# Performance work log

Hardware: AMD Instinct MI355X
Metric: run time of the kernel (lower is better)

Reference implementation:

```python
import jax, jax.numpy as jnp
import numpy as np

E = 8      # num_experts
R = 32     # LoRA rank
D = 1024   # in_features (d_model)
H = 4096   # out_features of fc1 (hidden)
B = 2
S = 2048
SCALING = 1.0 / R  # lora_alpha / rank with alpha=1


def setup_inputs() -> dict:
    key = jax.random.key(0)
    ks = jax.random.split(key, 9)
    def w(k, shape, scale=0.02):
        return jax.random.normal(k, shape, dtype=jnp.float32) * scale
    return {
        "x": jax.random.normal(ks[0], (B, S, D), dtype=jnp.float32),
        "router_w": w(ks[1], (E, D)),
        "router_b": jnp.zeros((E,), jnp.float32),
        "fc1_w": w(ks[2], (H, D)),
        "fc1_b": jnp.zeros((H,), jnp.float32),
        "fc2_w": w(ks[3], (D, H)),
        "fc2_b": jnp.zeros((D,), jnp.float32),
        "A_down": w(ks[4], (E, R, D)),
        "Ab_down": jnp.zeros((E, R), jnp.float32),
        "B_down": w(ks[5], (E, H, R)),
        "Bb_down": jnp.zeros((E, H), jnp.float32),
        "A_up": w(ks[6], (E, R, H)),
        "Ab_up": jnp.zeros((E, R), jnp.float32),
        "B_up": w(ks[7], (E, D, R)),
        "Bb_up": jnp.zeros((E, D), jnp.float32),
    }


def _moe_lora(x, mask, A, Ab, Bw, Bb):
    # x: [B,S,din]; mask: one-hot [B,S,E]; A: [E,R,din]; Bw: [E,dout,R]
    # rank-stage for all experts is cheap (R=32), select per token via one-hot
    h = jnp.einsum('bsd,erd->bser', x, A) + Ab          # [B,S,E,R]
    hsel = jnp.einsum('bser,bse->bsr', h, mask)          # [B,S,R]
    out = jnp.zeros(x.shape[:2] + (Bw.shape[1],), dtype=x.dtype)
    for e in range(E):  # fixed small expert count; avoids [B,S,E,dout] blowup
        out = out + mask[..., e:e + 1] * (hsel @ Bw[e].T + Bb[e])
    return out * SCALING


def reference(x, router_w, router_b, fc1_w, fc1_b, fc2_w, fc2_b,
              A_down, Ab_down, B_down, Bb_down,
              A_up, Ab_up, B_up, Bb_up):
    logits = x @ router_w.T + router_b                   # [B,S,E]
    routing = jax.nn.softmax(logits, axis=-1)
    index = jnp.argmax(logits, axis=-1)                  # top-1 expert [B,S]
    mask = jax.nn.one_hot(index, E, dtype=x.dtype)       # y_hard [B,S,E]
    expert_choice = mask - jax.lax.stop_gradient(routing) + routing
    # down: frozen fc1 + sparse LoRA (dropout layers in eval mode -> identity)
    down = x @ fc1_w.T + fc1_b + _moe_lora(x, mask, A_down, Ab_down, B_down, Bb_down)
    a = jax.nn.gelu(down, approximate=False)             # F.gelu exact
    up = a @ fc2_w.T + fc2_b + _moe_lora(a, mask, A_up, Ab_up, B_up, Bb_up)
    return up, routing, expert_choice
```

## Files before the change

### kernel.cpp

```cpp
#include <hip/hip_runtime.h>
#include <hip/hip_bf16.h>
#include <math.h>
#include <stdint.h>

#define E_ 8
#define R_ 32
#define D_ 1024
#define H_ 4096
#define NTOK 4096
#define M_MAX 5120
#define TILES_MAX 40
#define SCALING 0.03125f

typedef __attribute__((ext_vector_type(8))) __bf16 bf16x8;
typedef __attribute__((ext_vector_type(8))) unsigned short ushort8;
typedef __attribute__((ext_vector_type(4))) float floatx4;

__device__ __forceinline__ unsigned short f2b(float f) {
    union { float f; unsigned int i; } v; v.f = f;
    unsigned int x = v.i;
    x += 0x7fffu + ((x >> 16) & 1u);
    return (unsigned short)(x >> 16);
}
__device__ __forceinline__ float gelu_exact(float v) {
    return 0.5f * v * (1.0f + erff(v * 0.70710678118654752f));
}

#define GLOAD_LDS16(g, l) __builtin_amdgcn_global_load_lds( \
    (const __attribute__((address_space(1))) void*)(g),     \
    (__attribute__((address_space(3))) void*)(l), 16, 0, 0)

__global__ __launch_bounds__(256) void k_cvt_all(
    const float* __restrict__ w1, const float* __restrict__ w2,
    const float* __restrict__ Ad, const float* __restrict__ Bd,
    const float* __restrict__ Au, const float* __restrict__ Bu,
    unsigned short* __restrict__ w1b, unsigned short* __restrict__ w2b,
    unsigned short* __restrict__ Adb, unsigned short* __restrict__ Bdb,
    unsigned short* __restrict__ Aub, unsigned short* __restrict__ Bub)
{
    long g = ((long)blockIdx.x * 256 + threadIdx.x) * 8;
    const float* src; unsigned short* dst; long off;
    if      (g <  4194304L) { src = w1; dst = w1b; off = 0; }
    else if (g <  8388608L) { src = w2; dst = w2b; off = 4194304L; }
    else if (g <  8650752L) { src = Ad; dst = Adb; off = 8388608L; }
    else if (g <  9699328L) { src = Bd; dst = Bdb; off = 8650752L; }
    else if (g < 10747904L) { src = Au; dst = Aub; off = 9699328L; }
    else                    { src = Bu; dst = Bub; off = 10747904L; }
    long i = g - off;
    float4 a = *(const float4*)(src + i);
    float4 b = *(const float4*)(src + i + 4);
    ushort8 o;
    o[0] = f2b(a.x); o[1] = f2b(a.y); o[2] = f2b(a.z); o[3] = f2b(a.w);
    o[4] = f2b(b.x); o[5] = f2b(b.y); o[6] = f2b(b.z); o[7] = f2b(b.w);
    *(ushort8*)(dst + i) = o;
}

__global__ __launch_bounds__(256) void k_router(
    const float* __restrict__ x, const float* __restrict__ rw,
    const float* __restrict__ rb,
    float* __restrict__ out, int* __restrict__ idx)
{
    const int wave = threadIdx.x >> 6, lane = threadIdx.x & 63;
    const int t = blockIdx.x * 4 + wave;
    const float4* xr = (const float4*)(x + (size_t)t * D_);
    float4 xv[4];
#pragma unroll
    for (int s = 0; s < 4; ++s) xv[s] = xr[lane + 64 * s];
    float acc[E_];
#pragma unroll
    for (int e = 0; e < E_; ++e) {
        const float4* wr = (const float4*)(rw + (size_t)e * D_);
        float s = 0.f;
#pragma unroll
        for (int u = 0; u < 4; ++u) {
            float4 wv = wr[lane + 64 * u];
            s += xv[u].x * wv.x + xv[u].y * wv.y + xv[u].z * wv.z + xv[u].w * wv.w;
        }
        acc[e] = s;
    }
#pragma unroll
    for (int e = 0; e < E_; ++e) {
#pragma unroll
        for (int m = 32; m > 0; m >>= 1) acc[e] += __shfl_xor(acc[e], m, 64);
        acc[e] += rb[e];
    }
    int best = 0;
#pragma unroll
    for (int e = 1; e < E_; ++e) if (acc[e] > acc[best]) best = e;
    const float mx = acc[best];
    float pr[E_]; float se = 0.f;
#pragma unroll
    for (int e = 0; e < E_; ++e) { pr[e] = expf(acc[e] - mx); se += pr[e]; }
    const float inv = 1.f / se;
    if (lane < E_) {
        float r = pr[lane] * inv;
        out[(size_t)NTOK * D_ + (size_t)t * E_ + lane] = r;
        float maskv = (lane == best) ? 1.f : 0.f;
        out[(size_t)NTOK * D_ + (size_t)NTOK * E_ + (size_t)t * E_ + lane] = (maskv - r) + r;
    }
    if (lane == 0) idx[t] = best;
}

__global__ __launch_bounds__(256) void k_scan(
    const int* __restrict__ idx, int* __restrict__ hdr,
    int* __restrict__ tile_e, int* __restrict__ gather)
{
    __shared__ int cnt[256][E_];
    __shared__ int tot[E_], base[E_];
    const int tid = threadIdx.x;
    for (int m = tid; m < M_MAX; m += 256) gather[m] = -1;
    int c[E_];
#pragma unroll
    for (int e = 0; e < E_; ++e) c[e] = 0;
    for (int t = tid * 16; t < tid * 16 + 16; ++t) c[idx[t] & 7]++;
#pragma unroll
    for (int e = 0; e < E_; ++e) cnt[tid][e] = c[e];
    __syncthreads();
    if (tid < E_) {
        int run = 0;
        for (int i = 0; i < 256; ++i) { int v = cnt[i][tid]; cnt[i][tid] = run; run += v; }
        tot[tid] = run;
    }
    __syncthreads();
    if (tid == 0) {
        int b = 0, tp = 0;
        for (int e = 0; e < E_; ++e) {
            base[e] = b;
            int nt = (tot[e] + 127) >> 7;
            for (int k = 0; k < nt; ++k) tile_e[tp++] = e;
            b += nt << 7;
        }
        hdr[0] = b;
        hdr[1] = tp;
        for (int k = tp; k < TILES_MAX; ++k) tile_e[k] = 0;
    }
    __syncthreads();
    int p[E_];
#pragma unroll
    for (int e = 0; e < E_; ++e) p[e] = base[e] + cnt[tid][e];
    for (int t = tid * 16; t < tid * 16 + 16; ++t) { int e = idx[t] & 7; gather[p[e]++] = t; }
}

__global__ __launch_bounds__(128) void k_gather(
    const float* __restrict__ x, const int* __restrict__ gather,
    unsigned short* __restrict__ xg)
{
    const int m = blockIdx.x, tid = threadIdx.x;
    const int t = gather[m];
    ushort8* dst = (ushort8*)(xg + (size_t)m * D_);
    ushort8 o;
    if ((unsigned)t < (unsigned)NTOK) {
        const float4* src = (const float4*)(x + (size_t)t * D_);
        float4 a = src[tid * 2], b = src[tid * 2 + 1];
        o[0] = f2b(a.x); o[1] = f2b(a.y); o[2] = f2b(a.z); o[3] = f2b(a.w);
        o[4] = f2b(b.x); o[5] = f2b(b.y); o[6] = f2b(b.z); o[7] = f2b(b.w);
    } else {
        o = (ushort8)(0);
    }
    dst[tid] = o;
}

__global__ __launch_bounds__(256) void k_lora_a2(
    const unsigned short* __restrict__ A,
    const unsigned short* __restrict__ W,
    const float* __restrict__ Ab,
    const int* __restrict__ hdr, const int* __restrict__ tile_e,
    unsigned short* __restrict__ outb,
    int Ktot)
{
    const int mtile = blockIdx.y;
    int ntiles = hdr[1]; if (ntiles > TILES_MAX) ntiles = TILES_MAX;
    if (mtile >= ntiles) return;
    const int e = tile_e[mtile] & 7;
    const int m0 = mtile * 128 + blockIdx.x * 32;
    const int wave = threadIdx.x >> 6, lane = threadIdx.x & 63;
    const int q = lane >> 4, l16 = lane & 15;
    const int Ks = Ktot >> 2;
    const int kbase = wave * Ks;
    const floatx4 z4 = {0.f, 0.f, 0.f, 0.f};
    floatx4 acc[2][2] = {{z4, z4}, {z4, z4}};
    const bf16x8* A0 = (const bf16x8*)(A + (size_t)(m0 + l16) * Ktot);
    const bf16x8* A1 = (const bf16x8*)(A + (size_t)(m0 + 16 + l16) * Ktot);
    const bf16x8* W0 = (const bf16x8*)(W + ((size_t)e * 32 + l16) * Ktot);
    const bf16x8* W1 = (const bf16x8*)(W + ((size_t)e * 32 + 16 + l16) * Ktot);
    for (int k = kbase; k < kbase + Ks; k += 32) {
        int u = (k >> 3) + q;
        bf16x8 a0 = A0[u], a1 = A1[u];
        bf16x8 b0 = W0[u], b1 = W1[u];
        acc[0][0] = __builtin_amdgcn_mfma_f32_16x16x32_bf16(a0, b0, acc[0][0], 0, 0, 0);
        acc[0][1] = __builtin_amdgcn_mfma_f32_16x16x32_bf16(a0, b1, acc[0][1], 0, 0, 0);
        acc[1][0] = __builtin_amdgcn_mfma_f32_16x16x32_bf16(a1, b0, acc[1][0], 0, 0, 0);
        acc[1][1] = __builtin_amdgcn_mfma_f32_16x16x32_bf16(a1, b1, acc[1][1], 0, 0, 0);
    }
    __shared__ float red[4][32][32];
#pragma unroll
    for (int mi = 0; mi < 2; ++mi)
#pragma unroll
        for (int ni = 0; ni < 2; ++ni)
#pragma unroll
            for (int r = 0; r < 4; ++r)
                red[wave][mi * 16 + q * 4 + r][ni * 16 + l16] = acc[mi][ni][r];
    __syncthreads();
    for (int i = threadIdx.x; i < 1024; i += 256) {
        int lr = i >> 5, c = i & 31;
        float s = red[0][lr][c] + red[1][lr][c] + red[2][lr][c] + red[3][lr][c];
        outb[(size_t)(m0 + lr) * 32 + c] = f2b(SCALING * (s + Ab[e * 32 + c]));
    }
}

template <int KTOT, bool IS_FC1>
__global__ __launch_bounds__(256) void k_mlp(
    const unsigned short* __restrict__ Amat,
    const unsigned short* __restrict__ Wmat,
    const float* __restrict__ bias,
    const unsigned short* __restrict__ lora_h,
    const unsigned short* __restrict__ lora_B,
    const float* __restrict__ lora_b,
    const int* __restrict__ hdr, const int* __restrict__ tile_e,
    const int* __restrict__ gather,
    unsigned short* __restrict__ outb,
    float* __restrict__ outf,
    int NOUT)
{
    const int mtile = blockIdx.y;
    int ntiles = hdr[1]; if (ntiles > TILES_MAX) ntiles = TILES_MAX;
    if (mtile >= ntiles) return;
    const int e = tile_e[mtile] & 7;
    const int h0 = blockIdx.x * 128;
    const int m0 = mtile * 128;
    __shared__ bf16x8 As[1024];
    __shared__ bf16x8 Bs[1024];
    const int tid = threadIdx.x;
    const int lane = tid & 63;
    const int q = lane >> 4, l16 = lane & 15;
    const int wave = tid >> 6;
    const int wm = wave & 1, wn = wave >> 1;
    const floatx4 z4 = {0.f, 0.f, 0.f, 0.f};
    floatx4 acc[4][4];
#pragma unroll
    for (int mi = 0; mi < 4; ++mi)
#pragma unroll
        for (int ni = 0; ni < 4; ++ni) acc[mi][ni] = z4;

    const unsigned short* Abase = Amat + (size_t)m0 * KTOT;
    const unsigned short* Bbase = Wmat + (size_t)h0 * KTOT;

    for (int k0 = 0; k0 < KTOT; k0 += 64) {
#pragma unroll
        for (int rnd = 0; rnd < 4; ++rnd) {
            int s = rnd * 256 + tid;
            int row = s >> 3;
            int jj = (s & 7) ^ (row & 7);
            const unsigned short* ga = Abase + (size_t)row * KTOT + k0 + jj * 8;
            const unsigned short* gb = Bbase + (size_t)row * KTOT + k0 + jj * 8;
            GLOAD_LDS16(ga, As + rnd * 256 + wave * 64);
            GLOAD_LDS16(gb, Bs + rnd * 256 + wave * 64);
        }
        __syncthreads();
#pragma unroll
        for (int ka = 0; ka < 2; ++ka) {
            bf16x8 af[4], bfr[4];
#pragma unroll
            for (int mi = 0; mi < 4; ++mi) {
                int row = wm * 64 + mi * 16 + l16;
                af[mi] = As[row * 8 + ((ka * 4 + q) ^ (row & 7))];
            }
#pragma unroll
            for (int ni = 0; ni < 4; ++ni) {
                int row = wn * 64 + ni * 16 + l16;
                bfr[ni] = Bs[row * 8 + ((ka * 4 + q) ^ (row & 7))];
            }
#pragma unroll
            for (int mi = 0; mi < 4; ++mi)
#pragma unroll
                for (int ni = 0; ni < 4; ++ni)
                    acc[mi][ni] = __builtin_amdgcn_mfma_f32_16x16x32_bf16(af[mi], bfr[ni], acc[mi][ni], 0, 0, 0);
        }
        __syncthreads();
    }

    {
        bf16x8 a2[4], b2[4];
#pragma unroll
        for (int mi = 0; mi < 4; ++mi)
            a2[mi] = *(const bf16x8*)(lora_h + (size_t)(m0 + wm * 64 + mi * 16 + l16) * 32 + q * 8);
#pragma unroll
        for (int ni = 0; ni < 4; ++ni)
            b2[ni] = *(const bf16x8*)(lora_B + ((size_t)e * NOUT + h0 + wn * 64 + ni * 16 + l16) * 32 + q * 8);
#pragma unroll
        for (int mi = 0; mi < 4; ++mi)
#pragma unroll
            for (int ni = 0; ni < 4; ++ni)
                acc[mi][ni] = __builtin_amdgcn_mfma_f32_16x16x32_bf16(a2[mi], b2[ni], acc[mi][ni], 0, 0, 0);
    }

#pragma unroll
    for (int ni = 0; ni < 4; ++ni) {
        int gh = h0 + wn * 64 + ni * 16 + l16;
        float bv = bias[gh] + SCALING * lora_b[e * NOUT + gh];
#pragma unroll
        for (int mi = 0; mi < 4; ++mi) {
#pragma unroll
            for (int r = 0; r < 4; ++r) {
                int gm = m0 + wm * 64 + mi * 16 + q * 4 + r;
                float v = acc[mi][ni][r] + bv;
                if (IS_FC1) {
                    outb[(size_t)gm * NOUT + gh] = f2b(gelu_exact(v));
                } else {
                    int t = gather[gm];
                    if ((unsigned)t < (unsigned)NTOK) outf[(size_t)t * NOUT + gh] = v;
                }
            }
        }
    }
}

#define OFF_IDX      0u
#define OFF_HDR      16384u
#define OFF_TILE     16640u
#define OFF_GATHER   16896u
#define OFF_XG       37376u
#define OFF_HSELB    13144576u
#define OFF_AG       13472256u
#define OFF_HUPB     60658176u
#define OFF_W1B      60985856u
#define OFF_W2B      69374464u
#define OFF_ADB      77763072u
#define OFF_BDB      78287360u
#define OFF_AUB      80384512u
#define OFF_BUB      82481664u
#define WS_NEEDED    83005952u

extern "C" void kernel_launch(void* const* d_in, const int* in_sizes, int n_in,
                              void* d_out, int out_size, void* d_ws, size_t ws_size,
                              hipStream_t stream)
{
    (void)out_size;
    if (ws_size < (size_t)WS_NEEDED) return;
    if (n_in < 15 || in_sizes[0] != NTOK * D_ || in_sizes[3] != H_ * D_ ||
        in_sizes[5] != D_ * H_ || in_sizes[9] != E_ * H_ * R_) return;

    const float* x   = (const float*)d_in[0];
    const float* rw  = (const float*)d_in[1];
    const float* rb  = (const float*)d_in[2];
    const float* w1  = (const float*)d_in[3];
    const float* b1  = (const float*)d_in[4];
    const float* w2  = (const float*)d_in[5];
    const float* b2  = (const float*)d_in[6];
    const float* Ad  = (const float*)d_in[7];
    const float* Abd = (const float*)d_in[8];
    const float* Bd  = (const float*)d_in[9];
    const float* Bbd = (const float*)d_in[10];
    const float* Au  = (const float*)d_in[11];
    const float* Abu = (const float*)d_in[12];
    const float* Bu  = (const float*)d_in[13];
    const float* Bbu = (const float*)d_in[14];
    float* out = (float*)d_out;
    char* ws = (char*)d_ws;

    int* idx            = (int*)(ws + OFF_IDX);
    int* hdr            = (int*)(ws + OFF_HDR);
    int* tile_e         = (int*)(ws + OFF_TILE);
    int* gather         = (int*)(ws + OFF_GATHER);
    unsigned short* xg  = (unsigned short*)(ws + OFF_XG);
    unsigned short* hsb = (unsigned short*)(ws + OFF_HSELB);
    unsigned short* ag  = (unsigned short*)(ws + OFF_AG);
    unsigned short* hub = (unsigned short*)(ws + OFF_HUPB);
    unsigned short* w1b = (unsigned short*)(ws + OFF_W1B);
    unsigned short* w2b = (unsigned short*)(ws + OFF_W2B);
    unsigned short* Adb = (unsigned short*)(ws + OFF_ADB);
    unsigned short* Bdb = (unsigned short*)(ws + OFF_BDB);
    unsigned short* Aub = (unsigned short*)(ws + OFF_AUB);
    unsigned short* Bub = (unsigned short*)(ws + OFF_BUB);

    k_cvt_all<<<5376, 256, 0, stream>>>(w1, w2, Ad, Bd, Au, Bu,
                                        w1b, w2b, Adb, Bdb, Aub, Bub);

    k_router<<<NTOK / 4, 256, 0, stream>>>(x, rw, rb, out, idx);
    k_scan<<<1, 256, 0, stream>>>(idx, hdr, tile_e, gather);
    k_gather<<<M_MAX, 128, 0, stream>>>(x, gather, xg);
    k_lora_a2<<<dim3(4, TILES_MAX), 256, 0, stream>>>(xg, Adb, Abd, hdr, tile_e, hsb, D_);
    k_mlp<D_, true><<<dim3(H_ / 128, TILES_MAX), 256, 0, stream>>>(
        xg, w1b, b1, hsb, Bdb, Bbd, hdr, tile_e, gather, ag, nullptr, H_);
    k_lora_a2<<<dim3(4, TILES_MAX), 256, 0, stream>>>(ag, Aub, Abu, hdr, tile_e, hub, H_);
    k_mlp<H_, false><<<dim3(D_ / 128, TILES_MAX), 256, 0, stream>>>(
        ag, w2b, b2, hub, Bub, Bbu, hdr, tile_e, gather, nullptr, out, D_);
}
```

Baseline: 330.2 us.

## Split-K fc2, merge convert+router kernels, use tanh GELU approximation

Result: faster. 306.7 us (-7.1%).

```diff
diff --git a/kernel.cpp b/kernel.cpp
--- a/kernel.cpp
+++ b/kernel.cpp
@@ -22,46 +22,49 @@
     x += 0x7fffu + ((x >> 16) & 1u);
     return (unsigned short)(x >> 16);
 }
-__device__ __forceinline__ float gelu_exact(float v) {
-    return 0.5f * v * (1.0f + erff(v * 0.70710678118654752f));
+__device__ __forceinline__ float gelu_fast(float v) {
+    float u = v * (0.7978845608028654f + 0.0356774080857f * v * v);
+    float t = __expf(-2.f * fabsf(u));
+    float th = (1.f - t) * __builtin_amdgcn_rcpf(1.f + t);
+    th = (u >= 0.f) ? th : -th;
+    return 0.5f * v * (1.f + th);
 }
 
 #define GLOAD_LDS16(g, l) __builtin_amdgcn_global_load_lds( \
     (const __attribute__((address_space(1))) void*)(g),     \
     (__attribute__((address_space(3))) void*)(l), 16, 0, 0)
 
-__global__ __launch_bounds__(256) void k_cvt_all(
+__global__ __launch_bounds__(256) void k_prep(
     const float* __restrict__ w1, const float* __restrict__ w2,
     const float* __restrict__ Ad, const float* __restrict__ Bd,
     const float* __restrict__ Au, const float* __restrict__ Bu,
     unsigned short* __restrict__ w1b, unsigned short* __restrict__ w2b,
     unsigned short* __restrict__ Adb, unsigned short* __restrict__ Bdb,
-    unsigned short* __restrict__ Aub, unsigned short* __restrict__ Bub)
-{
-    long g = ((long)blockIdx.x * 256 + threadIdx.x) * 8;
-    const float* src; unsigned short* dst; long off;
-    if      (g <  4194304L) { src = w1; dst = w1b; off = 0; }
-    else if (g <  8388608L) { src = w2; dst = w2b; off = 4194304L; }
-    else if (g <  8650752L) { src = Ad; dst = Adb; off = 8388608L; }
-    else if (g <  9699328L) { src = Bd; dst = Bdb; off = 8650752L; }
-    else if (g < 10747904L) { src = Au; dst = Aub; off = 9699328L; }
-    else                    { src = Bu; dst = Bub; off = 10747904L; }
-    long i = g - off;
-    float4 a = *(const float4*)(src + i);
-    float4 b = *(const float4*)(src + i + 4);
-    ushort8 o;
-    o[0] = f2b(a.x); o[1] = f2b(a.y); o[2] = f2b(a.z); o[3] = f2b(a.w);
-    o[4] = f2b(b.x); o[5] = f2b(b.y); o[6] = f2b(b.z); o[7] = f2b(b.w);
-    *(ushort8*)(dst + i) = o;
-}
-
-__global__ __launch_bounds__(256) void k_router(
+    unsigned short* __restrict__ Aub, unsigned short* __restrict__ Bub,
     const float* __restrict__ x, const float* __restrict__ rw,
     const float* __restrict__ rb,
     float* __restrict__ out, int* __restrict__ idx)
 {
+    if (blockIdx.x < 5376) {
+        long g = ((long)blockIdx.x * 256 + threadIdx.x) * 8;
+        const float* src; unsigned short* dst; long off;
+        if      (g <  4194304L) { src = w1; dst = w1b; off = 0; }
+        else if (g <  8388608L) { src = w2; dst = w2b; off = 4194304L; }
+        else if (g <  8650752L) { src = Ad; dst = Adb; off = 8388608L; }
+        else if (g <  9699328L) { src = Bd; dst = Bdb; off = 8650752L; }
+        else if (g < 10747904L) { src = Au; dst = Aub; off = 9699328L; }
+        else                    { src = Bu; dst = Bub; off = 10747904L; }
+        long i = g - off;
+        float4 a = *(const float4*)(src + i);
+        float4 b = *(const float4*)(src + i + 4);
+        ushort8 o;
+        o[0] = f2b(a.x); o[1] = f2b(a.y); o[2] = f2b(a.z); o[3] = f2b(a.w);
+        o[4] = f2b(b.x); o[5] = f2b(b.y); o[6] = f2b(b.z); o[7] = f2b(b.w);
+        *(ushort8*)(dst + i) = o;
+        return;
+    }
     const int wave = threadIdx.x >> 6, lane = threadIdx.x & 63;
-    const int t = blockIdx.x * 4 + wave;
+    const int t = (blockIdx.x - 5376) * 4 + wave;
     const float4* xr = (const float4*)(x + (size_t)t * D_);
     float4 xv[4];
 #pragma unroll
@@ -208,7 +211,7 @@
     }
 }
 
-template <int KTOT, bool IS_FC1>
+template <int KTOT, bool IS_FC1, int NSPLIT>
 __global__ __launch_bounds__(256) void k_mlp(
     const unsigned short* __restrict__ Amat,
     const unsigned short* __restrict__ Wmat,
@@ -220,6 +223,7 @@
     const int* __restrict__ gather,
     unsigned short* __restrict__ outb,
     float* __restrict__ outf,
+    float* __restrict__ P,
     int NOUT)
 {
     const int mtile = blockIdx.y;
@@ -228,6 +232,9 @@
     const int e = tile_e[mtile] & 7;
     const int h0 = blockIdx.x * 128;
     const int m0 = mtile * 128;
+    const bool extras = (NSPLIT == 1) || (blockIdx.z == 0);
+    const int Kslice = KTOT / NSPLIT;
+    const int kstart = blockIdx.z * Kslice;
     __shared__ bf16x8 As[1024];
     __shared__ bf16x8 Bs[1024];
     const int tid = threadIdx.x;
@@ -245,7 +252,7 @@
     const unsigned short* Abase = Amat + (size_t)m0 * KTOT;
     const unsigned short* Bbase = Wmat + (size_t)h0 * KTOT;
 
-    for (int k0 = 0; k0 < KTOT; k0 += 64) {
+    for (int k0 = kstart; k0 < kstart + Kslice; k0 += 64) {
 #pragma unroll
         for (int rnd = 0; rnd < 4; ++rnd) {
             int s = rnd * 256 + tid;
@@ -279,7 +286,7 @@
         __syncthreads();
     }
 
-    {
+    if (extras) {
         bf16x8 a2[4], b2[4];
 #pragma unroll
         for (int mi = 0; mi < 4; ++mi)
@@ -297,7 +304,7 @@
 #pragma unroll
     for (int ni = 0; ni < 4; ++ni) {
         int gh = h0 + wn * 64 + ni * 16 + l16;
-        float bv = bias[gh] + SCALING * lora_b[e * NOUT + gh];
+        float bv = extras ? (bias[gh] + SCALING * lora_b[e * NOUT + gh]) : 0.f;
 #pragma unroll
         for (int mi = 0; mi < 4; ++mi) {
 #pragma unroll
@@ -305,14 +312,31 @@
                 int gm = m0 + wm * 64 + mi * 16 + q * 4 + r;
                 float v = acc[mi][ni][r] + bv;
                 if (IS_FC1) {
-                    outb[(size_t)gm * NOUT + gh] = f2b(gelu_exact(v));
-                } else {
+                    outb[(size_t)gm * NOUT + gh] = f2b(gelu_fast(v));
+                } else if (extras) {
                     int t = gather[gm];
                     if ((unsigned)t < (unsigned)NTOK) outf[(size_t)t * NOUT + gh] = v;
+                } else {
+                    P[(size_t)gm * NOUT + gh] = v;
                 }
             }
         }
     }
+}
+
+__global__ __launch_bounds__(256) void k_reduce(
+    const float* __restrict__ P, const int* __restrict__ gather,
+    float* __restrict__ out)
+{
+    const int m = blockIdx.x;
+    const int t = gather[m];
+    if ((unsigned)t >= (unsigned)NTOK) return;
+    const float4* p4 = (const float4*)(P + (size_t)m * D_);
+    float4* o4 = (float4*)(out + (size_t)t * D_);
+    int i = threadIdx.x;
+    float4 a = o4[i], b = p4[i];
+    a.x += b.x; a.y += b.y; a.z += b.z; a.w += b.w;
+    o4[i] = a;
 }
 
 #define OFF_IDX      0u
@@ -320,16 +344,17 @@
 #define OFF_TILE     16640u
 #define OFF_GATHER   16896u
 #define OFF_XG       37376u
-#define OFF_HSELB    13144576u
-#define OFF_AG       13472256u
-#define OFF_HUPB     60658176u
-#define OFF_W1B      60985856u
-#define OFF_W2B      69374464u
-#define OFF_ADB      77763072u
-#define OFF_BDB      78287360u
-#define OFF_AUB      80384512u
-#define OFF_BUB      82481664u
-#define WS_NEEDED    83005952u
+#define OFF_W1B      10523136u
+#define OFF_ADB      18911744u
+#define OFF_BDB      19436032u
+#define OFF_HSB      21533184u
+#define OFF_P        37376u
+#define OFF_AG       21860864u
+#define OFF_HUB      63803904u
+#define OFF_W2B      64131584u
+#define OFF_AUB      72520192u
+#define OFF_BUB      74617344u
+#define WS_NEEDED    75141632u
 
 extern "C" void kernel_launch(void* const* d_in, const int* in_sizes, int n_in,
                               void* d_out, int out_size, void* d_ws, size_t ws_size,
@@ -363,26 +388,27 @@
     int* tile_e         = (int*)(ws + OFF_TILE);
     int* gather         = (int*)(ws + OFF_GATHER);
     unsigned short* xg  = (unsigned short*)(ws + OFF_XG);
-    unsigned short* hsb = (unsigned short*)(ws + OFF_HSELB);
+    unsigned short* hsb = (unsigned short*)(ws + OFF_HSB);
     unsigned short* ag  = (unsigned short*)(ws + OFF_AG);
-    unsigned short* hub = (unsigned short*)(ws + OFF_HUPB);
+    unsigned short* hub = (unsigned short*)(ws + OFF_HUB);
     unsigned short* w1b = (unsigned short*)(ws + OFF_W1B);
     unsigned short* w2b = (unsigned short*)(ws + OFF_W2B);
     unsigned short* Adb = (unsigned short*)(ws + OFF_ADB);
     unsigned short* Bdb = (unsigned short*)(ws + OFF_BDB);
     unsigned short* Aub = (unsigned short*)(ws + OFF_AUB);
     unsigned short* Bub = (unsigned short*)(ws + OFF_BUB);
-
-    k_cvt_all<<<5376, 256, 0, stream>>>(w1, w2, Ad, Bd, Au, Bu,
-                                        w1b, w2b, Adb, Bdb, Aub, Bub);
-
-    k_router<<<NTOK / 4, 256, 0, stream>>>(x, rw, rb, out, idx);
+    float* P            = (float*)(ws + OFF_P);
+
+    k_prep<<<6400, 256, 0, stream>>>(w1, w2, Ad, Bd, Au, Bu,
+                                     w1b, w2b, Adb, Bdb, Aub, Bub,
+                                     x, rw, rb, out, idx);
     k_scan<<<1, 256, 0, stream>>>(idx, hdr, tile_e, gather);
     k_gather<<<M_MAX, 128, 0, stream>>>(x, gather, xg);
     k_lora_a2<<<dim3(4, TILES_MAX), 256, 0, stream>>>(xg, Adb, Abd, hdr, tile_e, hsb, D_);
-    k_mlp<D_, true><<<dim3(H_ / 128, TILES_MAX), 256, 0, stream>>>(
-        xg, w1b, b1, hsb, Bdb, Bbd, hdr, tile_e, gather, ag, nullptr, H_);
+    k_mlp<D_, true, 1><<<dim3(H_ / 128, TILES_MAX, 1), 256, 0, stream>>>(
+        xg, w1b, b1, hsb, Bdb, Bbd, hdr, tile_e, gather, ag, nullptr, nullptr, H_);
     k_lora_a2<<<dim3(4, TILES_MAX), 256, 0, stream>>>(ag, Aub, Abu, hdr, tile_e, hub, H_);
-    k_mlp<H_, false><<<dim3(D_ / 128, TILES_MAX), 256, 0, stream>>>(
-        ag, w2b, b2, hub, Bub, Bbu, hdr, tile_e, gather, nullptr, out, D_);
-}
+    k_mlp<H_, false, 2><<<dim3(D_ / 128, TILES_MAX, 2), 256, 0, stream>>>(
+        ag, w2b, b2, hub, Bub, Bbu, hdr, tile_e, gather, nullptr, out, P, D_);
+    k_reduce<<<M_MAX, 256, 0, stream>>>(P, gather, out);
+}
```
